# Kernel tuning notes

Measured on AMD Instinct MI355X. Metric: run time of the kernel, lower is better.

## Reference

```python
import jax, jax.numpy as jnp
import numpy as np

N_NODES = 100000


def _gcn_layer(x, W, b, src, dst, n):
    # symmetric normalization (add_self_loops=False): deg = in-degree at dst
    deg = jax.ops.segment_sum(jnp.ones_like(src, dtype=x.dtype), dst, num_segments=n)
    dis = jnp.where(deg > 0, jax.lax.rsqrt(jnp.maximum(deg, 1.0)), 0.0)
    h = x @ W                                    # [N, out]
    norm = dis[src] * dis[dst]                   # [E]
    msg = h[src] * norm[:, None]                 # [E, out]
    out = jax.ops.segment_sum(msg, dst, num_segments=n)
    return out + b


def setup_inputs() -> dict:
    key = jax.random.key(0)
    k1, k2, k3, k4, k5, k6 = jax.random.split(key, 6)
    F_IN, HID, OUT = 64, 64, 2
    x = jax.random.normal(k1, (N_NODES, F_IN), dtype=jnp.float32)
    edge_index = jax.random.randint(k2, (2, 1600000), 0, N_NODES, dtype=jnp.int64)
    s1 = 1.0 / np.sqrt(2 * F_IN)
    s2 = 1.0 / np.sqrt(HID)
    W1 = jax.random.uniform(k3, (2 * F_IN, HID), jnp.float32, -s1, s1)
    b1 = jax.random.uniform(k4, (HID,), jnp.float32, -s1, s1)
    W2 = jax.random.uniform(k5, (HID, OUT), jnp.float32, -s2, s2)
    b2 = jax.random.uniform(k6, (OUT,), jnp.float32, -s2, s2)
    return {"x": x, "edge_index": edge_index, "W1": W1, "b1": b1, "W2": W2, "b2": b2}


def reference(x, edge_index, W1, b1, W2, b2):
    n = x.shape[0]
    src, dst = edge_index[0], edge_index[1]
    # global mean pool broadcast to every node, concat on feature dim -> [N, 2F]
    mean = jnp.mean(x, axis=0, keepdims=True)
    complete = jnp.concatenate([x, jnp.broadcast_to(mean, x.shape)], axis=1)
    h = _gcn_layer(complete, W1, b1, src, dst, n)
    h = jax.nn.relu(h)
    out = _gcn_layer(h, W2, b2, src, dst, n)
    return out
```

## Files before the change

kernel.cpp:

```cpp
#include <hip/hip_runtime.h>


#define NPB        256
#define NPB_SHIFT  8
#define BKTS       512
#define BKT_CAP    5120
#define CHUNK      4096
#define EPT        8
#define CS_BLK     64
#define CUR_STRIDE 32

using bf16x8 = __attribute__((ext_vector_type(8))) short;
using f32x4  = __attribute__((ext_vector_type(4))) float;

__device__ __forceinline__ unsigned short f2bf(float v) {
    unsigned u = __float_as_uint(v);
    u += 0x7FFFu + ((u >> 16) & 1u);
    return (unsigned short)(u >> 16);
}
__device__ __forceinline__ float bfu_lo(unsigned u) { return __uint_as_float(u << 16); }
__device__ __forceinline__ float bfu_hi(unsigned u) { return __uint_as_float(u & 0xFFFF0000u); }

__global__ __launch_bounds__(512) void bucketAC_kernel(
        const int* __restrict__ src, const int* __restrict__ dst,
        int e, unsigned* __restrict__ pairs, int* __restrict__ cursor,
        const float* __restrict__ x, float* __restrict__ sums,
        const float* __restrict__ W1, unsigned short* __restrict__ wtg, int n) {
    int tid = threadIdx.x;
    if (blockIdx.x < CS_BLK) {
        __shared__ float4 s4[512];
        int cb = blockIdx.x;
        const float4* x4 = (const float4*)x;
        int total4 = n * 16;
        float4 acc = make_float4(0.f, 0.f, 0.f, 0.f);
        for (int i = cb * 512 + tid; i < total4; i += CS_BLK * 512) {
            float4 v = x4[i];
            acc.x += v.x; acc.y += v.y; acc.z += v.z; acc.w += v.w;
        }
        s4[tid] = acc;
        __syncthreads();
        if (tid < 16) {
            float4 v = s4[tid];
            for (int k = 1; k < 32; ++k) {
                float4 w = s4[tid + 16 * k];
                v.x += w.x; v.y += w.y; v.z += w.z; v.w += w.w;
            }
            atomicAdd(&sums[tid * 4 + 0], v.x);
            atomicAdd(&sums[tid * 4 + 1], v.y);
            atomicAdd(&sums[tid * 4 + 2], v.z);
            atomicAdd(&sums[tid * 4 + 3], v.w);
        }
        return;
    }
    if (blockIdx.x == CS_BLK) {
        for (int i = tid; i < 4096; i += 512) {
            int k = i >> 6, j = i & 63;
            wtg[j * 64 + k] = f2bf(W1[k * 64 + j]);
        }
        return;
    }
    __shared__ int cnt[BKTS], sb[BKTS], gpos[BKTS];
    __shared__ unsigned stage[CHUNK];
    __shared__ unsigned short bb[CHUNK];
    int chunkStart = (blockIdx.x - CS_BLK - 1) * CHUNK;
    int v = e - chunkStart;
    if (v > CHUNK) v = CHUNK;
    cnt[tid] = 0;
    __syncthreads();
    int myb[EPT], myoff[EPT];
    unsigned myp[EPT];
#pragma unroll
    for (int t = 0; t < EPT; ++t) {
        int i = chunkStart + t * 512 + tid;
        myb[t] = -1;
        if (i < e) {
            int s = src[i], d = dst[i];
            myb[t] = d >> NPB_SHIFT;
            myp[t] = ((unsigned)s << NPB_SHIFT) | (unsigned)(d & (NPB - 1));
            myoff[t] = atomicAdd(&cnt[myb[t]], 1);
        }
    }
    __syncthreads();
    sb[tid] = cnt[tid];
    __syncthreads();
    for (int off = 1; off < BKTS; off <<= 1) {
        int t = (tid >= off) ? sb[tid - off] : 0;
        __syncthreads();
        sb[tid] += t;
        __syncthreads();
    }
    {
        int excl = tid ? sb[tid - 1] : 0;
        int cb = cnt[tid];
        if (cb > 0) {
            int gb = atomicAdd(&cursor[tid * CUR_STRIDE], cb);
            gpos[tid] = tid * BKT_CAP + gb - excl;
        }
        cnt[tid] = excl;
    }
    __syncthreads();
#pragma unroll
    for (int t = 0; t < EPT; ++t) {
        if (myb[t] >= 0) {
            int p = cnt[myb[t]] + myoff[t];
            stage[p] = myp[t];
            bb[p] = (unsigned short)myb[t];
        }
    }
    __syncthreads();
    for (int j = tid; j < v; j += 512) {
        int bk = bb[j];
        int wi = gpos[bk] + j;
        if (wi < (bk + 1) * BKT_CAP) pairs[wi] = stage[j];
    }
}

__global__ __launch_bounds__(512) void csrBG_kernel(
        const unsigned* __restrict__ pairs, const int* __restrict__ cursor,
        float* __restrict__ dis, int* __restrict__ rowstart,
        int* __restrict__ eidx, int n,
        const float* __restrict__ sums, const float* __restrict__ W1,
        const unsigned short* __restrict__ wtg, const float* __restrict__ x,
        unsigned short* __restrict__ h1s) {
    __shared__ int ldeg[NPB];
    __shared__ int lcur[NPB];
    __shared__ int scanbuf[512];
    __shared__ int s_ebase;
    __shared__ __align__(16) float cv[64];
    __shared__ unsigned short Ws[64 * 72];
    __shared__ unsigned short Xs[2][64 * 72];
    float* disl = (float*)ldeg;
    int b = blockIdx.x;
    int tid = threadIdx.x;
    int node0 = b << NPB_SHIFT;
    int nl = n - node0;
    if (nl > NPB) nl = NPB;
    int cnt_b = cursor[b * CUR_STRIDE];
    if (cnt_b > BKT_CAP) cnt_b = BKT_CAP;
    if (tid < NPB) ldeg[tid] = 0;
    if (tid == 0) s_ebase = 0;
    __syncthreads();
    if (tid < b) atomicAdd(&s_ebase, cursor[tid * CUR_STRIDE]);
    const unsigned* mp = pairs + (size_t)b * BKT_CAP;
    for (int i = tid; i < cnt_b; i += 512)
        atomicAdd(&ldeg[mp[i] & (NPB - 1)], 1);
    __syncthreads();
    scanbuf[tid] = (tid < NPB) ? ldeg[tid] : 0;
    __syncthreads();
    for (int off = 1; off < 512; off <<= 1) {
        int t = (tid >= off) ? scanbuf[tid - off] : 0;
        __syncthreads();
        scanbuf[tid] += t;
        __syncthreads();
    }
    int ebase = s_ebase;
    int mydeg = 0;
    if (tid < NPB) {
        int ex = tid ? scanbuf[tid - 1] : 0;
        lcur[tid] = ex;
        mydeg = ldeg[tid];
        if (tid < nl) rowstart[node0 + tid] = ebase + ex;
    }
    if (tid == 0 && node0 + NPB >= n)
        rowstart[n] = ebase + cnt_b;
    __syncthreads();
    if (tid < NPB) {
        float dv = mydeg > 0 ? rsqrtf((float)mydeg) : 0.f;
        disl[tid] = dv;
        if (tid < nl) dis[node0 + tid] = dv;
    }
    for (int i = tid; i < cnt_b; i += 512) {
        unsigned p = mp[i];
        int pos = atomicAdd(&lcur[p & (NPB - 1)], 1);
        eidx[ebase + pos] = (int)(p >> NPB_SHIFT);
    }
    if (tid < 64) {
        float inv_n = 1.0f / (float)n;
        float acc = 0.f;
        for (int k = 0; k < 64; ++k) acc += (sums[k] * inv_n) * W1[(64 + k) * 64 + tid];
        cv[tid] = acc;
    }
    for (int i = tid; i < 1024; i += 512) {
        int j = i >> 4, k4 = (i & 15) * 4;
        *(ushort4*)&Ws[j * 72 + k4] = *(const ushort4*)&wtg[j * 64 + k4];
    }
    int lane = tid & 63;
    int wv = tid >> 6;
    int tile = wv >> 2;
    int w4 = wv & 3;
    int l15 = lane & 15;
    int quad = lane >> 4;
#pragma unroll
    for (int it = 0; it < 2; ++it) {
        __syncthreads();
        for (int i = tid; i < 2048; i += 512) {
            int r = i >> 4, k4 = (i & 15) * 4;
            int gr = node0 + it * 128 + r;
            float4 xv = make_float4(0.f, 0.f, 0.f, 0.f);
            if (gr < n) xv = *(const float4*)&x[(size_t)gr * 64 + k4];
            ushort4 hv;
            hv.x = f2bf(xv.x); hv.y = f2bf(xv.y); hv.z = f2bf(xv.z); hv.w = f2bf(xv.w);
            *(ushort4*)&Xs[r >> 6][(r & 63) * 72 + k4] = hv;
        }
        __syncthreads();
        int xrow = w4 * 16 + l15;
        f32x4 acc0 = {0.f, 0.f, 0.f, 0.f}, acc1 = acc0, acc2 = acc0, acc3 = acc0;
#pragma unroll
        for (int ks = 0; ks < 2; ++ks) {
            bf16x8 bfrag = *(const bf16x8*)&Xs[tile][xrow * 72 + ks * 32 + quad * 8];
            bf16x8 a0 = *(const bf16x8*)&Ws[(0 * 16 + l15) * 72 + ks * 32 + quad * 8];
            bf16x8 a1 = *(const bf16x8*)&Ws[(1 * 16 + l15) * 72 + ks * 32 + quad * 8];
            bf16x8 a2 = *(const bf16x8*)&Ws[(2 * 16 + l15) * 72 + ks * 32 + quad * 8];
            bf16x8 a3 = *(const bf16x8*)&Ws[(3 * 16 + l15) * 72 + ks * 32 + quad * 8];
            acc0 = __builtin_amdgcn_mfma_f32_16x16x32_bf16(a0, bfrag, acc0, 0, 0, 0);
            acc1 = __builtin_amdgcn_mfma_f32_16x16x32_bf16(a1, bfrag, acc1, 0, 0, 0);
            acc2 = __builtin_amdgcn_mfma_f32_16x16x32_bf16(a2, bfrag, acc2, 0, 0, 0);
            acc3 = __builtin_amdgcn_mfma_f32_16x16x32_bf16(a3, bfrag, acc3, 0, 0, 0);
        }
        int lrow = it * 128 + tile * 64 + xrow;
        int grow = node0 + lrow;
        if (grow < n) {
            float dv = disl[lrow];
            const float4* c4 = (const float4*)cv;
            f32x4 accs[4] = {acc0, acc1, acc2, acc3};
#pragma unroll
            for (int t = 0; t < 4; ++t) {
                float4 cj = c4[t * 4 + quad];
                ushort4 hs;
                hs.x = f2bf((accs[t][0] + cj.x) * dv);
                hs.y = f2bf((accs[t][1] + cj.y) * dv);
                hs.z = f2bf((accs[t][2] + cj.z) * dv);
                hs.w = f2bf((accs[t][3] + cj.w) * dv);
                *(ushort4*)&h1s[(size_t)grow * 64 + t * 16 + quad * 4] = hs;
            }
        }
    }
}

__global__ void gather1_kernel(const int* __restrict__ rowstart,
                               const int* __restrict__ eidx, const float* __restrict__ dis,
                               const unsigned short* __restrict__ h1s,
                               const float* __restrict__ b1, const float* __restrict__ W2,
                               float* __restrict__ h2s, int n) {
    int lane = threadIdx.x & 63;
    int node = blockIdx.x * 4 + (threadIdx.x >> 6);
    if (node >= n) return;
    int rs = rowstart[node];
    int re = rowstart[node + 1];
    int dn = re - rs;
    int m = dn < 64 ? dn : 64;
    int eHeld = (lane < m) ? eidx[rs + lane] : 0;
    int sub = lane >> 5;
    int fp  = (lane & 31) * 2;
    float ax = 0.f, ay = 0.f;
    int j = 0;
    for (; j + 16 <= m; j += 16) {
        int s0 = __shfl(eHeld, j + 0 + sub, 64);
        int s1 = __shfl(eHeld, j + 2 + sub, 64);
        int s2 = __shfl(eHeld, j + 4 + sub, 64);
        int s3 = __shfl(eHeld, j + 6 + sub, 64);
        int s4 = __shfl(eHeld, j + 8 + sub, 64);
        int s5 = __shfl(eHeld, j + 10 + sub, 64);
        int s6 = __shfl(eHeld, j + 12 + sub, 64);
        int s7 = __shfl(eHeld, j + 14 + sub, 64);
        unsigned u0 = *(const unsigned*)&h1s[((size_t)s0 << 6) + fp];
        unsigned u1 = *(const unsigned*)&h1s[((size_t)s1 << 6) + fp];
        unsigned u2 = *(const unsigned*)&h1s[((size_t)s2 << 6) + fp];
        unsigned u3 = *(const unsigned*)&h1s[((size_t)s3 << 6) + fp];
        unsigned u4 = *(const unsigned*)&h1s[((size_t)s4 << 6) + fp];
        unsigned u5 = *(const unsigned*)&h1s[((size_t)s5 << 6) + fp];
        unsigned u6 = *(const unsigned*)&h1s[((size_t)s6 << 6) + fp];
        unsigned u7 = *(const unsigned*)&h1s[((size_t)s7 << 6) + fp];
        ax += (bfu_lo(u0) + bfu_lo(u1)) + (bfu_lo(u2) + bfu_lo(u3))
            + (bfu_lo(u4) + bfu_lo(u5)) + (bfu_lo(u6) + bfu_lo(u7));
        ay += (bfu_hi(u0) + bfu_hi(u1)) + (bfu_hi(u2) + bfu_hi(u3))
            + (bfu_hi(u4) + bfu_hi(u5)) + (bfu_hi(u6) + bfu_hi(u7));
    }
    for (; j + 8 <= m; j += 8) {
        int s0 = __shfl(eHeld, j + 0 + sub, 64);
        int s1 = __shfl(eHeld, j + 2 + sub, 64);
        int s2 = __shfl(eHeld, j + 4 + sub, 64);
        int s3 = __shfl(eHeld, j + 6 + sub, 64);
        unsigned u0 = *(const unsigned*)&h1s[((size_t)s0 << 6) + fp];
        unsigned u1 = *(const unsigned*)&h1s[((size_t)s1 << 6) + fp];
        unsigned u2 = *(const unsigned*)&h1s[((size_t)s2 << 6) + fp];
        unsigned u3 = *(const unsigned*)&h1s[((size_t)s3 << 6) + fp];
        ax += (bfu_lo(u0) + bfu_lo(u1)) + (bfu_lo(u2) + bfu_lo(u3));
        ay += (bfu_hi(u0) + bfu_hi(u1)) + (bfu_hi(u2) + bfu_hi(u3));
    }
    for (; j + 4 <= m; j += 4) {
        int s0 = __shfl(eHeld, j + 0 + sub, 64);
        int s1 = __shfl(eHeld, j + 2 + sub, 64);
        unsigned u0 = *(const unsigned*)&h1s[((size_t)s0 << 6) + fp];
        unsigned u1 = *(const unsigned*)&h1s[((size_t)s1 << 6) + fp];
        ax += bfu_lo(u0) + bfu_lo(u1);
        ay += bfu_hi(u0) + bfu_hi(u1);
    }
    for (; j < m; j += 2) {
        int jj = j + sub;
        int s = __shfl(eHeld, jj < m ? jj : 0, 64);
        if (jj < m) {
            unsigned u = *(const unsigned*)&h1s[((size_t)s << 6) + fp];
            ax += bfu_lo(u);
            ay += bfu_hi(u);
        }
    }
    for (int t = 64; t < dn; ++t) {
        if (sub == 0) {
            int s = eidx[rs + t];
            unsigned u = *(const unsigned*)&h1s[((size_t)s << 6) + fp];
            ax += bfu_lo(u);
            ay += bfu_hi(u);
        }
    }
    ax += __shfl_xor(ax, 32, 64);
    ay += __shfl_xor(ay, 32, 64);
    float di = dis[node];
    float2 bv = ((const float2*)b1)[lane & 31];
    float4 w = ((const float4*)W2)[lane & 31];
    float t0 = fmaxf(di * ax + bv.x, 0.f);
    float t1 = fmaxf(di * ay + bv.y, 0.f);
    float v0 = t0 * w.x + t1 * w.z;
    float v1 = t0 * w.y + t1 * w.w;
#pragma unroll
    for (int off = 1; off <= 16; off <<= 1) {
        v0 += __shfl_xor(v0, off, 64);
        v1 += __shfl_xor(v1, off, 64);
    }
    if (lane == 0) {
        h2s[(size_t)node * 2 + 0] = di * v0;
        h2s[(size_t)node * 2 + 1] = di * v1;
    }
}

__global__ void gather2_kernel(const int* __restrict__ rowstart,
                               const int* __restrict__ eidx, const float* __restrict__ dis,
                               const float2* __restrict__ h2s, const float* __restrict__ b2,
                               float2* __restrict__ out, int n) {
    int tid = threadIdx.x;
    int node = blockIdx.x * 16 + (tid >> 4);
    if (node >= n) return;
    int el = tid & 15;
    int rs = rowstart[node];
    int dn = rowstart[node + 1] - rs;
    float ax = 0.f, ay = 0.f;
    for (int t = el; t < dn; t += 16) {
        int s = eidx[rs + t];
        float2 h = h2s[s];
        ax += h.x;
        ay += h.y;
    }
#pragma unroll
    for (int off = 1; off <= 8; off <<= 1) {
        ax += __shfl_xor(ax, off, 64);
        ay += __shfl_xor(ay, off, 64);
    }
    if (el == 0) {
        float di = dis[node];
        out[node] = make_float2(di * ax + b2[0], di * ay + b2[1]);
    }
}

extern "C" void kernel_launch(void* const* d_in, const int* in_sizes, int n_in,
                              void* d_out, int out_size, void* d_ws, size_t ws_size,
                              hipStream_t stream) {
    const float* x  = (const float*)d_in[0];
    const int*   ei = (const int*)d_in[1];
    const float* W1 = (const float*)d_in[2];
    const float* b1 = (const float*)d_in[3];
    const float* W2 = (const float*)d_in[4];
    const float* b2 = (const float*)d_in[5];
    float2* out = (float2*)d_out;

    const int n = in_sizes[0] / 64;
    const int e = in_sizes[1] / 2;
    const int* srcI = ei;
    const int* dstI = ei + e;
    const int nbkt = (n + NPB - 1) >> NPB_SHIFT;

    char* p = (char*)d_ws;
    int* rowstart = (int*)p;    p += ((size_t)(n + 1) * 4 + 255) & ~255ull;
    float* dis    = (float*)p;  p += ((size_t)n * 4 + 255) & ~255ull;
    float* sums   = (float*)p;
    int* cursor   = (int*)(p + 256);
    size_t zsize  = 256 + (size_t)nbkt * CUR_STRIDE * 4;
    char* zbase   = p;          p += (zsize + 255) & ~255ull;
    unsigned short* wtg = (unsigned short*)p;  p += (4096 * 2 + 255) & ~255ull;
    int* eidx     = (int*)p;    p += ((size_t)e * 4 + 255) & ~255ull;
    unsigned* pairs = (unsigned*)p;  p += ((size_t)nbkt * BKT_CAP * 4 + 255) & ~255ull;
    unsigned short* h1s = (unsigned short*)p;  p += ((size_t)n * 64 * 2 + 255) & ~255ull;
    float* h2s    = (float*)p;

    hipMemsetAsync(zbase, 0, zsize, stream);

    const int nchunks = (e + CHUNK - 1) / CHUNK;

    bucketAC_kernel<<<CS_BLK + 1 + nchunks, 512, 0, stream>>>(srcI, dstI, e, pairs, cursor,
                                                              x, sums, W1, wtg, n);
    csrBG_kernel<<<nbkt, 512, 0, stream>>>(pairs, cursor, dis, rowstart, eidx, n,
                                           sums, W1, wtg, x, h1s);
    gather1_kernel<<<(n + 3) / 4, 256, 0, stream>>>(rowstart, eidx, dis, h1s, b1, W2, h2s, n);
    gather2_kernel<<<(n + 15) / 16, 256, 0, stream>>>(rowstart, eidx, dis, (const float2*)h2s,
                                                      b2, out, n);
}
```

Measured before the change: 186.1 us.

## Replace LDS Hillis-Steele scans with wave-shuffle scans and prestage bf16 x

Replaces the barrier-heavy shared-memory prefix scans in both the bucketing and CSR kernels with wavefront shuffle scans plus a small cross-wave combine, and computes the ebase with a shuffle reduction instead of shared atomics. The column-sum blocks now also write a bf16 copy of x, and the CSR/GEMM kernel loads that 8-wide bf16 copy instead of converting fp32 itself. CS_BLK is doubled to spread the extra conversion work. The bf16 copy costs an extra write and read of x in exchange for halving the GEMM tile load traffic.

```diff
diff --git a/kernel.cpp b/kernel.cpp
--- a/kernel.cpp
+++ b/kernel.cpp
@@ -7,7 +7,7 @@
 #define BKT_CAP    5120
 #define CHUNK      4096
 #define EPT        8
-#define CS_BLK     64
+#define CS_BLK     128
 #define CUR_STRIDE 32
 
 using bf16x8 = __attribute__((ext_vector_type(8))) short;
@@ -25,7 +25,8 @@
         const int* __restrict__ src, const int* __restrict__ dst,
         int e, unsigned* __restrict__ pairs, int* __restrict__ cursor,
         const float* __restrict__ x, float* __restrict__ sums,
-        const float* __restrict__ W1, unsigned short* __restrict__ wtg, int n) {
+        const float* __restrict__ W1, unsigned short* __restrict__ wtg,
+        unsigned short* __restrict__ xbf, int n) {
     int tid = threadIdx.x;
     if (blockIdx.x < CS_BLK) {
         __shared__ float4 s4[512];
@@ -36,6 +37,9 @@
         for (int i = cb * 512 + tid; i < total4; i += CS_BLK * 512) {
             float4 v = x4[i];
             acc.x += v.x; acc.y += v.y; acc.z += v.z; acc.w += v.w;
+            ushort4 hv;
+            hv.x = f2bf(v.x); hv.y = f2bf(v.y); hv.z = f2bf(v.z); hv.w = f2bf(v.w);
+            *(ushort4*)&xbf[(size_t)i * 4] = hv;
         }
         s4[tid] = acc;
         __syncthreads();
@@ -59,7 +63,8 @@
         }
         return;
     }
-    __shared__ int cnt[BKTS], sb[BKTS], gpos[BKTS];
+    __shared__ int cnt[BKTS], gpos[BKTS];
+    __shared__ int wsumA[8];
     __shared__ unsigned stage[CHUNK];
     __shared__ unsigned short bb[CHUNK];
     int chunkStart = (blockIdx.x - CS_BLK - 1) * CHUNK;
@@ -81,23 +86,25 @@
         }
     }
     __syncthreads();
-    sb[tid] = cnt[tid];
-    __syncthreads();
-    for (int off = 1; off < BKTS; off <<= 1) {
-        int t = (tid >= off) ? sb[tid - off] : 0;
-        __syncthreads();
-        sb[tid] += t;
-        __syncthreads();
-    }
-    {
-        int excl = tid ? sb[tid - 1] : 0;
-        int cb = cnt[tid];
-        if (cb > 0) {
-            int gb = atomicAdd(&cursor[tid * CUR_STRIDE], cb);
-            gpos[tid] = tid * BKT_CAP + gb - excl;
-        }
-        cnt[tid] = excl;
-    }
+    int lane = tid & 63, wvi = tid >> 6;
+    int myCnt = cnt[tid];
+    int sv = myCnt;
+#pragma unroll
+    for (int off = 1; off < 64; off <<= 1) {
+        int t = __shfl_up(sv, off, 64);
+        if (lane >= off) sv += t;
+    }
+    if (lane == 63) wsumA[wvi] = sv;
+    __syncthreads();
+    int wbase = 0;
+#pragma unroll
+    for (int k = 0; k < 8; ++k) if (k < wvi) wbase += wsumA[k];
+    int excl = sv + wbase - myCnt;
+    if (myCnt > 0) {
+        int gb = atomicAdd(&cursor[tid * CUR_STRIDE], myCnt);
+        gpos[tid] = tid * BKT_CAP + gb - excl;
+    }
+    cnt[tid] = excl;
     __syncthreads();
 #pragma unroll
     for (int t = 0; t < EPT; ++t) {
@@ -120,55 +127,60 @@
         float* __restrict__ dis, int* __restrict__ rowstart,
         int* __restrict__ eidx, int n,
         const float* __restrict__ sums, const float* __restrict__ W1,
-        const unsigned short* __restrict__ wtg, const float* __restrict__ x,
+        const unsigned short* __restrict__ wtg, const unsigned short* __restrict__ xbf,
         unsigned short* __restrict__ h1s) {
     __shared__ int ldeg[NPB];
     __shared__ int lcur[NPB];
-    __shared__ int scanbuf[512];
-    __shared__ int s_ebase;
+    __shared__ int wred[8], wsum[8];
     __shared__ __align__(16) float cv[64];
     __shared__ unsigned short Ws[64 * 72];
     __shared__ unsigned short Xs[2][64 * 72];
     float* disl = (float*)ldeg;
     int b = blockIdx.x;
     int tid = threadIdx.x;
+    int lane = tid & 63;
+    int wvi = tid >> 6;
     int node0 = b << NPB_SHIFT;
     int nl = n - node0;
     if (nl > NPB) nl = NPB;
     int cnt_b = cursor[b * CUR_STRIDE];
     if (cnt_b > BKT_CAP) cnt_b = BKT_CAP;
     if (tid < NPB) ldeg[tid] = 0;
-    if (tid == 0) s_ebase = 0;
-    __syncthreads();
-    if (tid < b) atomicAdd(&s_ebase, cursor[tid * CUR_STRIDE]);
+    int c = (tid < b) ? cursor[tid * CUR_STRIDE] : 0;
+#pragma unroll
+    for (int off = 1; off < 64; off <<= 1) c += __shfl_xor(c, off, 64);
+    if (lane == 0) wred[wvi] = c;
+    __syncthreads();
     const unsigned* mp = pairs + (size_t)b * BKT_CAP;
     for (int i = tid; i < cnt_b; i += 512)
         atomicAdd(&ldeg[mp[i] & (NPB - 1)], 1);
-    __syncthreads();
-    scanbuf[tid] = (tid < NPB) ? ldeg[tid] : 0;
-    __syncthreads();
-    for (int off = 1; off < 512; off <<= 1) {
-        int t = (tid >= off) ? scanbuf[tid - off] : 0;
-        __syncthreads();
-        scanbuf[tid] += t;
-        __syncthreads();
-    }
-    int ebase = s_ebase;
-    int mydeg = 0;
+    int ebase = 0;
+#pragma unroll
+    for (int k = 0; k < 8; ++k) ebase += wred[k];
+    __syncthreads();
+    int mydeg = (tid < NPB) ? ldeg[tid] : 0;
+    int sv = mydeg;
+#pragma unroll
+    for (int off = 1; off < 64; off <<= 1) {
+        int t = __shfl_up(sv, off, 64);
+        if (lane >= off) sv += t;
+    }
+    if (lane == 63) wsum[wvi] = sv;
+    __syncthreads();
+    int wbase = 0;
+#pragma unroll
+    for (int k = 0; k < 8; ++k) if (k < wvi) wbase += wsum[k];
+    int excl = sv + wbase - mydeg;
     if (tid < NPB) {
-        int ex = tid ? scanbuf[tid - 1] : 0;
-        lcur[tid] = ex;
-        mydeg = ldeg[tid];
-        if (tid < nl) rowstart[node0 + tid] = ebase + ex;
-    }
-    if (tid == 0 && node0 + NPB >= n)
-        rowstart[n] = ebase + cnt_b;
-    __syncthreads();
-    if (tid < NPB) {
+        lcur[tid] = excl;
+        if (tid < nl) rowstart[node0 + tid] = ebase + excl;
         float dv = mydeg > 0 ? rsqrtf((float)mydeg) : 0.f;
         disl[tid] = dv;
         if (tid < nl) dis[node0 + tid] = dv;
     }
+    if (tid == 0 && node0 + NPB >= n)
+        rowstart[n] = ebase + cnt_b;
+    __syncthreads();
     for (int i = tid; i < cnt_b; i += 512) {
         unsigned p = mp[i];
         int pos = atomicAdd(&lcur[p & (NPB - 1)], 1);
@@ -184,8 +196,7 @@
         int j = i >> 4, k4 = (i & 15) * 4;
         *(ushort4*)&Ws[j * 72 + k4] = *(const ushort4*)&wtg[j * 64 + k4];
     }
-    int lane = tid & 63;
-    int wv = tid >> 6;
+    int wv = wvi;
     int tile = wv >> 2;
     int w4 = wv & 3;
     int l15 = lane & 15;
@@ -193,14 +204,12 @@
 #pragma unroll
     for (int it = 0; it < 2; ++it) {
         __syncthreads();
-        for (int i = tid; i < 2048; i += 512) {
-            int r = i >> 4, k4 = (i & 15) * 4;
+        for (int i = tid; i < 1024; i += 512) {
+            int r = i >> 3, c8 = (i & 7) * 8;
             int gr = node0 + it * 128 + r;
-            float4 xv = make_float4(0.f, 0.f, 0.f, 0.f);
-            if (gr < n) xv = *(const float4*)&x[(size_t)gr * 64 + k4];
-            ushort4 hv;
-            hv.x = f2bf(xv.x); hv.y = f2bf(xv.y); hv.z = f2bf(xv.z); hv.w = f2bf(xv.w);
-            *(ushort4*)&Xs[r >> 6][(r & 63) * 72 + k4] = hv;
+            bf16x8 hv = {0, 0, 0, 0, 0, 0, 0, 0};
+            if (gr < n) hv = *(const bf16x8*)&xbf[(size_t)gr * 64 + c8];
+            *(bf16x8*)&Xs[r >> 6][(r & 63) * 72 + c8] = hv;
         }
         __syncthreads();
         int xrow = w4 * 16 + l15;
@@ -386,6 +395,7 @@
     size_t zsize  = 256 + (size_t)nbkt * CUR_STRIDE * 4;
     char* zbase   = p;          p += (zsize + 255) & ~255ull;
     unsigned short* wtg = (unsigned short*)p;  p += (4096 * 2 + 255) & ~255ull;
+    unsigned short* xbf = (unsigned short*)p;  p += ((size_t)n * 64 * 2 + 255) & ~255ull;
     int* eidx     = (int*)p;    p += ((size_t)e * 4 + 255) & ~255ull;
     unsigned* pairs = (unsigned*)p;  p += ((size_t)nbkt * BKT_CAP * 4 + 255) & ~255ull;
     unsigned short* h1s = (unsigned short*)p;  p += ((size_t)n * 64 * 2 + 255) & ~255ull;
@@ -396,9 +406,9 @@
     const int nchunks = (e + CHUNK - 1) / CHUNK;
 
     bucketAC_kernel<<<CS_BLK + 1 + nchunks, 512, 0, stream>>>(srcI, dstI, e, pairs, cursor,
-                                                              x, sums, W1, wtg, n);
+                                                              x, sums, W1, wtg, xbf, n);
     csrBG_kernel<<<nbkt, 512, 0, stream>>>(pairs, cursor, dis, rowstart, eidx, n,
-                                           sums, W1, wtg, x, h1s);
+                                           sums, W1, wtg, xbf, h1s);
     gather1_kernel<<<(n + 3) / 4, 256, 0, stream>>>(rowstart, eidx, dis, h1s, b1, W2, h2s, n);
     gather2_kernel<<<(n + 15) / 16, 256, 0, stream>>>(rowstart, eidx, dis, (const float2*)h2s,
                                                       b2, out, n);
```

After: 182.5 us. Within noise of the previous version (-1.9%).
